# Kernel optimization log

Measured on AMD Instinct MI355X. Metric: run time of the kernel, lower is better.

Reference implementation:

```python
import jax, jax.numpy as jnp
import numpy as np

H, W = 512, 1024
NUM_CLASSES = 19
N_THING = 8
CENTER_THRESHOLD = 0.1
NMS_KERNEL = 7
KEEP_K = 128


def setup_inputs() -> dict:
    key = jax.random.key(0)
    k1, k2, k3 = jax.random.split(key, 3)
    return {
        "semantic_logits": jax.random.normal(k1, (1, H, W, NUM_CLASSES), jnp.float32),
        "center_heatmap": jax.random.uniform(k2, (H, W, 1), dtype=jnp.float32),
        "center_offsets": jax.random.normal(k3, (H, W, 2), jnp.float32) * 8.0,
        "thing_class_ids": jnp.arange(N_THING, dtype=jnp.int32),
    }


def _nms_heatmap(center_heatmap):
    # threshold, then keep only local maxima of a k x k max-pool (zero-padded;
    # -inf init is equivalent since thresholded values are >= 0)
    hm = jnp.where(center_heatmap > CENTER_THRESHOLD, center_heatmap, 0.0)  # [H,W,1]
    pooled = jax.lax.reduce_window(hm, -jnp.inf, jax.lax.max,
                                   (NMS_KERNEL, NMS_KERNEL, 1), (1, 1, 1), 'SAME')
    hm = jnp.where(pooled == hm, hm, 0.0)
    return hm[..., 0]  # [H,W]


def reference(semantic_logits, center_heatmap, center_offsets, thing_class_ids):
    # semantic prediction [H,W] (batch=1, like the TF merge path)
    semantic = jnp.argmax(semantic_logits, axis=-1).astype(jnp.int32)[0]
    thing_mask = (semantic[..., None] == thing_class_ids[None, None, :]).any(-1)  # [H,W] bool

    hm = _nms_heatmap(center_heatmap)                     # [H,W]
    scores, idx = jax.lax.top_k(hm.reshape(-1), KEEP_K)   # fixed-K centers
    valid = scores > 0.0                                  # [K]
    cy = (idx // W).astype(jnp.float32)
    cx = (idx % W).astype(jnp.float32)
    centers = jnp.stack([cy, cx], axis=-1)                # [K,2] (y,x)

    # center-per-pixel = pixel coord + predicted offset
    yy, xx = jnp.meshgrid(jnp.arange(H, dtype=jnp.float32),
                          jnp.arange(W, dtype=jnp.float32), indexing='ij')
    cpp = (jnp.stack([yy, xx], axis=-1) + center_offsets).reshape(-1, 2)  # [HW,2]

    # squared euclidean distance (argmin-equivalent to tf.norm), matmul form
    d2 = ((centers ** 2).sum(-1)[:, None]
          - 2.0 * centers @ cpp.T
          + (cpp ** 2).sum(-1)[None, :])                  # [K,HW]
    d2 = jnp.where(valid[:, None], d2, jnp.inf)           # mask padded centers
    assign = jnp.argmin(d2, axis=0).reshape(H, W)         # closest center index

    instance_seg = (assign.astype(jnp.int32) + 1) * thing_mask.astype(jnp.int32)
    score_map = scores[assign] * thing_mask.astype(jnp.float32)
    return instance_seg, hm, score_map, semantic
```

## Files before the change

kernel.cpp:

```cpp
#include <hip/hip_runtime.h>

#define HH 512
#define WW 1024
#define HWSZ (HH*WW)
#define NCLS 19
#define KEEP 128
#define CTHR 0.1f
#define NBLK 512
#define NRED 16
#define SEGPB 32
#define GSLOT 192
#define PRODOFF (1 + NRED)
typedef unsigned int u32;
typedef unsigned long long u64;

static __device__ __forceinline__ int key_bin2k(u64 k) {
    unsigned u = (unsigned)(k >> 32);
    if (u >= 0x3F000000u) {
        int b = 1024 + (int)((u - 0x3F000000u) >> 13);
        return b > 2047 ? 2047 : b;
    }
    return (int)(u >> 21);
}

static __device__ __forceinline__ int lds_push(int* cnt, bool want, int lane, u64 lmask_lt) {
    u64 mask = __ballot(want);
    int pos = -1;
    if (mask) {
        int leader = __builtin_ctzll(mask);
        int bpos = 0;
        if (lane == leader) bpos = atomicAdd(cnt, (int)__popcll(mask));
        bpos = __shfl(bpos, leader);
        if (want) pos = bpos + (int)__popcll(mask & lmask_lt);
    }
    return pos;
}

static __device__ __forceinline__ void bitonic_lds(u64* b, int m, int tid) {
    for (int kk = 2; kk <= m; kk <<= 1) {
        for (int j = kk >> 1; j; j >>= 1) {
            for (int i = tid; i < m; i += 256) {
                int ixj = i ^ j;
                if (ixj > i) {
                    bool desc = ((i & kk) == 0);
                    u64 a = b[i], c = b[ixj];
                    if ((a < c) == desc) { b[i] = c; b[ixj] = a; }
                }
            }
            __syncthreads();
        }
    }
}

static __device__ __forceinline__ void bitonic256_reg(u64* ov, int tid) {
    u64 a = ov[tid];
    __syncthreads();
    for (int kk = 2; kk <= 256; kk <<= 1) {
        bool desc = ((tid & kk) == 0);
        for (int j = kk >> 1; j; j >>= 1) {
            u64 b;
            if (j >= 64) {
                ov[tid] = a; __syncthreads();
                b = ov[tid ^ j]; __syncthreads();
            } else {
                b = __shfl_xor(a, j);
            }
            bool up = ((tid & j) == 0);
            bool keepMax = (up == desc);
            a = keepMax ? (a > b ? a : b) : (a < b ? a : b);
        }
    }
    ov[tid] = a;
    __syncthreads();
}

static __device__ __forceinline__ int cutoff2k(unsigned* hist, unsigned* cs, int tid,
                                               int* s_bin, int* s_K) {
    if (tid == 0) *s_bin = 2048;
    unsigned c = 0;
#pragma unroll
    for (int i = 0; i < 8; i++) c += hist[tid * 8 + i];
    cs[tid] = c;
    __syncthreads();
    for (int d = 1; d < 256; d <<= 1) {
        unsigned v = cs[tid];
        unsigned w = (tid + d < 256) ? cs[tid + d] : 0u;
        __syncthreads();
        cs[tid] = v + w;
        __syncthreads();
    }
    if (tid == 0) *s_K = (int)cs[0] < KEEP ? (int)cs[0] : KEEP;
    __syncthreads();
    int K = *s_K;
    unsigned above = (tid < 255) ? cs[tid + 1] : 0u;
    if (K > 0 && above < (unsigned)K && (unsigned)K <= cs[tid]) {
        unsigned acc = above;
        for (int b = 7; b >= 0; b--) {
            unsigned h = hist[tid * 8 + b];
            if (acc + h >= (unsigned)K) { *s_bin = tid * 8 + b; break; }
            acc += h;
        }
    }
    __syncthreads();
    return *s_bin;
}

__global__ void __launch_bounds__(256) pipeline_kernel(
        const float* __restrict__ heat, float* __restrict__ hm_out,
        u64* __restrict__ keys, u32* __restrict__ tagarr, u32* __restrict__ cntarr,
        u64* __restrict__ gtop, u32* __restrict__ gcnt, u32* __restrict__ tag2arr,
        int maxpb, float4* __restrict__ centers)
{
    __shared__ __align__(16) char smem[33792];
    __shared__ int scnt2[SEGPB];
    __shared__ int s_lcnt, s_m, s_bin, s_K, s_out;

    int tid = threadIdx.x, lane = tid & 63;
    u64 lmask_lt = (1ull << lane) - 1ull;

    if (blockIdx.x >= PRODOFF) {
        const int TX = 64, TY = 16;
        float* sin_ = (float*)smem;
        float* shm  = (float*)(smem + 6160);
        u64*   lk   = (u64*)(smem + 11792);
        int t = blockIdx.x - PRODOFF;
        if (tid == 0) s_lcnt = 0;
        int bx = t & 15, by = t >> 4;
        int ox = bx * TX, oy = by * TY;

        for (int i = tid; i < 22 * 70; i += 256) {
            int ly = i / 70, lx = i % 70;
            int gy = oy + ly - 3, gx = ox + lx - 3;
            float v = 0.f;
            if (gy >= 0 && gy < HH && gx >= 0 && gx < WW) {
                float tt = heat[gy * WW + gx];
                v = (tt > CTHR) ? tt : 0.f;
            }
            sin_[i] = v;
        }
        __syncthreads();
        for (int i = tid; i < 22 * 64; i += 256) {
            int ly = i >> 6, lx = i & 63;
            float m = sin_[ly * 70 + lx];
#pragma unroll
            for (int d = 1; d < 7; d++) m = fmaxf(m, sin_[ly * 70 + lx + d]);
            shm[i] = m;
        }
        __syncthreads();
        for (int i = tid; i < 16 * 64; i += 256) {
            int ly = i >> 6, lx = i & 63;
            float m = shm[i];
#pragma unroll
            for (int d = 1; d < 7; d++) m = fmaxf(m, shm[(ly + d) * 64 + lx]);
            float c = sin_[(ly + 3) * 70 + lx + 3];
            float o = (m == c) ? c : 0.f;
            int gy = oy + ly, gx = ox + lx;
            hm_out[gy * WW + gx] = o;
            if (o > 0.f) {
                int pos = atomicAdd(&s_lcnt, 1);
                lk[pos] = ((u64)__float_as_uint(o) << 32) |
                          (u64)(0xFFFFFFFFu - (unsigned)(gy * WW + gx));
            }
        }
        __syncthreads();
        int n = s_lcnt < maxpb ? s_lcnt : maxpb;
        for (int i = tid; i < n; i += 256)
            keys[(size_t)i * NBLK + t] = lk[i];
        __syncthreads();
        if (tid == 0) {
            __hip_atomic_store(&cntarr[t], (u32)n, __ATOMIC_RELAXED, __HIP_MEMORY_SCOPE_AGENT);
            __hip_atomic_store(&tagarr[t], 1u, __ATOMIC_RELEASE, __HIP_MEMORY_SCOPE_AGENT);
        }
        return;
    }

    u64* kbuf = (u64*)smem;
    unsigned* hist = (unsigned*)(smem + 24576);
    unsigned* cs   = (unsigned*)(smem + 32768);

    if (blockIdx.x >= 1) {
        int r = blockIdx.x - 1, g0 = r * SEGPB;
        if (tid < SEGPB) {
            while (__hip_atomic_load(&tagarr[g0 + tid], __ATOMIC_RELAXED,
                                     __HIP_MEMORY_SCOPE_AGENT) != 1u)
                __builtin_amdgcn_s_sleep(8);
        }
        __syncthreads();
        if (tid == 0) __threadfence();
        __syncthreads();
        if (tid < SEGPB) {
            int c = (int)cntarr[g0 + tid];
            scnt2[tid] = c < 0 ? 0 : (c > maxpb ? maxpb : c);
        }
        if (tid == 0) s_m = 0;
        { uint4* h4 = (uint4*)hist; for (int i = tid; i < 512; i += 256) h4[i] = make_uint4(0,0,0,0); }
        __syncthreads();
        int mxc = 0;
        for (int j = 0; j < SEGPB; j++) { int c = scnt2[j]; mxc = c > mxc ? c : mxc; }
        int nslots = SEGPB * mxc;

        for (int base = 0; base < nslots; base += 1024) {
            u64 kv[4]; bool pv[4];
#pragma unroll
            for (int u = 0; u < 4; u++) {
                int i = base + u * 256 + tid;
                int sg = i & (SEGPB - 1), sl = i >> 5;
                pv[u] = (i < nslots) && (sl < scnt2[sg]);
                kv[u] = pv[u] ? keys[(size_t)sl * NBLK + (g0 + sg)] : 0ull;
            }
#pragma unroll
            for (int u = 0; u < 4; u++)
                if (pv[u]) atomicAdd(&hist[key_bin2k(kv[u])], 1u);
        }
        __syncthreads();
        int cb = cutoff2k(hist, cs, tid, &s_bin, &s_K);

        for (int base = 0; base < nslots; base += 1024) {
#pragma unroll
            for (int u = 0; u < 4; u++) {
                int i = base + u * 256 + tid;
                int sg = i & (SEGPB - 1), sl = i >> 5;
                bool pv = (i < nslots) && (sl < scnt2[sg]);
                u64 kv = pv ? keys[(size_t)sl * NBLK + (g0 + sg)] : 0ull;
                bool want = pv && key_bin2k(kv) >= cb;
                int pos = lds_push(&s_m, want, lane, lmask_lt);
                if (want) kbuf[pos] = kv;
            }
        }
        __syncthreads();
        int n = s_m;
        if (n <= GSLOT) {
            for (int i = tid; i < n; i += 256) gtop[r * GSLOT + i] = kbuf[i];
            if (tid == 0) s_out = n;
        } else {
            int m = 256; while (m < n) m <<= 1;
            for (int i = tid; i < m; i += 256) if (i >= n) kbuf[i] = 0ull;
            __syncthreads();
            if (m == 256) bitonic256_reg(kbuf, tid); else bitonic_lds(kbuf, m, tid);
            if (tid < KEEP) gtop[r * GSLOT + tid] = kbuf[tid];
            if (tid == 0) s_out = KEEP;
        }
        __syncthreads();
        if (tid == 0) {
            __hip_atomic_store(&gcnt[r], (u32)s_out, __ATOMIC_RELAXED, __HIP_MEMORY_SCOPE_AGENT);
            __hip_atomic_store(&tag2arr[r], 1u, __ATOMIC_RELEASE, __HIP_MEMORY_SCOPE_AGENT);
        }
        return;
    }

    if (tid < NRED) {
        while (__hip_atomic_load(&tag2arr[tid], __ATOMIC_RELAXED,
                                 __HIP_MEMORY_SCOPE_AGENT) != 1u)
            __builtin_amdgcn_s_sleep(8);
    }
    __syncthreads();
    if (tid == 0) __threadfence();
    __syncthreads();
    if (tid < NRED) {
        int c = (int)gcnt[tid];
        scnt2[tid] = c < 0 ? 0 : (c > GSLOT ? GSLOT : c);
    }
    if (tid == 0) s_m = 0;
    { uint4* h4 = (uint4*)hist; for (int i = tid; i < 512; i += 256) h4[i] = make_uint4(0,0,0,0); }
    __syncthreads();

    const int nslots = NRED * GSLOT;
    for (int base = 0; base < nslots; base += 1024) {
        u64 kv[4]; bool pv[4];
#pragma unroll
        for (int u = 0; u < 4; u++) {
            int i = base + u * 256 + tid;
            int b = i / GSLOT, j = i - b * GSLOT;
            pv[u] = (j < scnt2[b]);
            kv[u] = pv[u] ? gtop[i] : 0ull;
        }
#pragma unroll
        for (int u = 0; u < 4; u++)
            if (pv[u]) atomicAdd(&hist[key_bin2k(kv[u])], 1u);
    }
    __syncthreads();
    int cb = cutoff2k(hist, cs, tid, &s_bin, &s_K);

    for (int base = 0; base < nslots; base += 1024) {
#pragma unroll
        for (int u = 0; u < 4; u++) {
            int i = base + u * 256 + tid;
            int b = i / GSLOT, j = i - b * GSLOT;
            bool pv = (j < scnt2[b]);
            u64 kv = pv ? gtop[i] : 0ull;
            bool want = pv && key_bin2k(kv) >= cb;
            int pos = lds_push(&s_m, want, lane, lmask_lt);
            if (want) kbuf[pos] = kv;
        }
    }
    __syncthreads();
    int n = s_m;
    int m = 256; while (m < n) m <<= 1;
    for (int i = tid; i < m; i += 256) if (i >= n) kbuf[i] = 0ull;
    __syncthreads();
    if (m == 256) bitonic256_reg(kbuf, tid); else bitonic_lds(kbuf, m, tid);

    if (tid < KEEP) {
        u64 k64 = kbuf[tid];
        float sc_, cy, cx, a;
        if (k64 == 0ull) { sc_ = 0.f; cy = 0.f; cx = 0.f; a = 0.f; }
        else {
            sc_ = __uint_as_float((unsigned)(k64 >> 32));
            unsigned idx = 0xFFFFFFFFu - (unsigned)(k64 & 0xFFFFFFFFu);
            cy = (float)(idx / WW);
            cx = (float)(idx % WW);
            a = cy * cy + cx * cx;
        }
        centers[tid] = make_float4(cy, cx, a, sc_);
    }
    __hip_atomic_store(&tagarr[2 * tid],     0u, __ATOMIC_RELAXED, __HIP_MEMORY_SCOPE_AGENT);
    __hip_atomic_store(&tagarr[2 * tid + 1], 0u, __ATOMIC_RELAXED, __HIP_MEMORY_SCOPE_AGENT);
    if (tid < NRED)
        __hip_atomic_store(&tag2arr[tid], 0u, __ATOMIC_RELAXED, __HIP_MEMORY_SCOPE_AGENT);
}

__global__ void __launch_bounds__(256) assign_kernel(
        const float* __restrict__ logits, const float* __restrict__ offs,
        const int* __restrict__ thing_ids, int n_thing,
        const float4* __restrict__ centers, float* __restrict__ out)
{
    __shared__ float4 sc[KEEP];
    __shared__ float4 skept[KEEP];
    __shared__ int   skidx[KEEP];
    __shared__ float slog[256 * NCLS];
    __shared__ float sred[16];
    __shared__ float ured[4];
    __shared__ int   wcnt[4];
    __shared__ int   s_nkept;
    __shared__ int   sids[32];

    int tid = threadIdx.x;
    if (tid < KEEP) sc[tid] = centers[tid];
    if (tid < n_thing) sids[tid] = thing_ids[tid];

    int bx = blockIdx.x & 63;
    int by = blockIdx.x >> 6;
    int lr = tid >> 4, lc = tid & 15;
    int gy = by * 16 + lr, gx = bx * 16 + lc;
    int p  = gy * WW + gx;

    {
        const float4* src4 = (const float4*)(logits + ((size_t)(by * 16) * WW + bx * 16) * NCLS);
        float4* dst4 = (float4*)slog;
        for (int i = tid; i < 16 * 76; i += 256) {
            int r = i / 76, cidx = i % 76;
            dst4[i] = src4[(size_t)r * 4864 + cidx];
        }
    }

    float2 off2 = ((const float2*)offs)[p];
    float py = __fadd_rn((float)gy, off2.x);
    float px = __fadd_rn((float)gx, off2.y);

    float ymn = py, ymx = py, xmn = px, xmx = px;
    for (int d = 32; d; d >>= 1) {
        ymn = fminf(ymn, __shfl_xor(ymn, d));
        ymx = fmaxf(ymx, __shfl_xor(ymx, d));
        xmn = fminf(xmn, __shfl_xor(xmn, d));
        xmx = fmaxf(xmx, __shfl_xor(xmx, d));
    }
    if ((tid & 63) == 0) {
        int w = tid >> 6;
        sred[w * 4 + 0] = ymn; sred[w * 4 + 1] = ymx;
        sred[w * 4 + 2] = xmn; sred[w * 4 + 3] = xmx;
    }
    __syncthreads();

    ymn = fminf(fminf(sred[0], sred[4]), fminf(sred[8],  sred[12]));
    ymx = fmaxf(fmaxf(sred[1], sred[5]), fmaxf(sred[9],  sred[13]));
    xmn = fminf(fminf(sred[2], sred[6]), fminf(sred[10], sred[14]));
    xmx = fmaxf(fmaxf(sred[3], sred[7]), fmaxf(sred[11], sred[15]));

    float L = INFINITY, U = INFINITY;
    bool valid = false;
    if (tid < KEEP) {
        float4 c4 = sc[tid];
        valid = (c4.w > 0.f);
        if (valid) {
            float dyl = fmaxf(fmaxf(ymn - c4.x, c4.x - ymx), 0.f);
            float dxl = fmaxf(fmaxf(xmn - c4.y, c4.y - xmx), 0.f);
            L = dyl * dyl + dxl * dxl;
            float dyu = fmaxf(fabsf(c4.x - ymn), fabsf(c4.x - ymx));
            float dxu = fmaxf(fabsf(c4.y - xmn), fabsf(c4.y - xmx));
            U = dyu * dyu + dxu * dxu;
        }
    }
    float u = U;
    for (int d = 32; d; d >>= 1) u = fminf(u, __shfl_xor(u, d));
    if ((tid & 63) == 0) ured[tid >> 6] = u;
    __syncthreads();
    float Umin = fminf(fminf(ured[0], ured[1]), fminf(ured[2], ured[3]));

    bool keep = valid && (L <= Umin + 8.0f);
    u64 mask = __ballot(keep);
    int lane = tid & 63;
    int prefix = __popcll(mask & ((1ull << lane) - 1ull));
    if (lane == 0) wcnt[tid >> 6] = __popcll(mask);
    __syncthreads();
    int base = (tid >> 6) == 1 ? wcnt[0] : 0;
    if (keep) { skept[base + prefix] = sc[tid]; skidx[base + prefix] = tid; }
    if (tid == 0) s_nkept = wcnt[0] + wcnt[1];
    __syncthreads();

    const float* l = slog + tid * NCLS;
    float best = l[0];
    int cls = 0;
#pragma unroll
    for (int cc = 1; cc < NCLS; cc++) {
        float v = l[cc];
        if (v > best) { best = v; cls = cc; }
    }
    bool thing = false;
    for (int j = 0; j < n_thing; j++) thing = thing || (cls == sids[j]);

    float b = __fadd_rn(__fmul_rn(py, py), __fmul_rn(px, px));

    float bestd = INFINITY;
    int bi = -1;
    int nk = s_nkept;
    for (int k = 0; k < nk; k++) {
        float4 c4 = skept[k];
        float m  = __fmaf_rn(c4.y, px, __fmul_rn(c4.x, py));
        float d2 = __fadd_rn(__fsub_rn(c4.z, __fadd_rn(m, m)), b);
        if (d2 < bestd) { bestd = d2; bi = k; }
    }

    float inst, smap;
    if (bi < 0) { inst = thing ? 1.f : 0.f; smap = 0.f; }
    else {
        inst = thing ? (float)(skidx[bi] + 1) : 0.f;
        smap = thing ? skept[bi].w : 0.f;
    }
    out[p] = inst;
    out[2 * HWSZ + p] = smap;
    out[3 * HWSZ + p] = (float)cls;
}

extern "C" void kernel_launch(void* const* d_in, const int* in_sizes, int n_in,
                              void* d_out, int out_size, void* d_ws, size_t ws_size,
                              hipStream_t stream) {
    const float* logits = (const float*)d_in[0];
    const float* heat   = (const float*)d_in[1];
    const float* offs   = (const float*)d_in[2];
    const int*   tids   = (const int*)d_in[3];
    int n_thing = in_sizes[3];
    if (n_thing > 32) n_thing = 32;

    float* out = (float*)d_out;
    char* ws = (char*)d_ws;
    u32* tagarr  = (u32*)ws;
    u32* tag2arr = (u32*)(ws + 2048);
    u32* cntarr  = (u32*)(ws + 4096);
    u32* gcnt    = (u32*)(ws + 6144);
    float4* centers = (float4*)(ws + 8192);
    u64* gtop = (u64*)(ws + 16384);
    long long avail = (long long)ws_size - 65536;
    int maxpb = (int)(avail / (NBLK * 8));
    if (maxpb > 96) maxpb = 96;
    if (maxpb < 16) maxpb = 16;
    u64* keys = (u64*)(ws + 65536);

    pipeline_kernel<<<dim3(NBLK + PRODOFF), dim3(256), 0, stream>>>(
        heat, out + HWSZ, keys, tagarr, cntarr, gtop, gcnt, tag2arr, maxpb, centers);
    assign_kernel<<<dim3(2048), dim3(256), 0, stream>>>(
        logits, offs, tids, n_thing, centers, out);
}
```

Measured before the change: 51.20 us.

## Fuse assign stage into producer blocks of a single persistent mega-kernel

```diff
diff --git a/kernel.cpp b/kernel.cpp
--- a/kernel.cpp
+++ b/kernel.cpp
@@ -10,7 +10,7 @@
 #define NRED 16
 #define SEGPB 32
 #define GSLOT 192
-#define PRODOFF (1 + NRED)
+#define WOFF (1 + NRED)
 typedef unsigned int u32;
 typedef unsigned long long u64;
 
@@ -105,26 +105,36 @@
     return *s_bin;
 }
 
-__global__ void __launch_bounds__(256) pipeline_kernel(
-        const float* __restrict__ heat, float* __restrict__ hm_out,
-        u64* __restrict__ keys, u32* __restrict__ tagarr, u32* __restrict__ cntarr,
+__global__ void __launch_bounds__(256) mega_kernel(
+        const float* __restrict__ logits, const float* __restrict__ heat,
+        const float* __restrict__ offs, const int* __restrict__ thing_ids, int n_thing,
+        float* __restrict__ out, u64* __restrict__ keys,
+        u32* __restrict__ tagarr, u32* __restrict__ cntarr,
         u64* __restrict__ gtop, u32* __restrict__ gcnt, u32* __restrict__ tag2arr,
-        int maxpb, float4* __restrict__ centers)
+        u32* __restrict__ wflags, u32* __restrict__ centersw, int maxpb)
 {
     __shared__ __align__(16) char smem[33792];
     __shared__ int scnt2[SEGPB];
-    __shared__ int s_lcnt, s_m, s_bin, s_K, s_out;
-
-    int tid = threadIdx.x, lane = tid & 63;
+    __shared__ int s_lcnt, s_m, s_bin, s_K, s_out, s_nkept;
+    __shared__ float sred[16];
+    __shared__ float ured[4];
+    __shared__ int wcnt[4];
+    __shared__ int sids[32];
+    __shared__ float4 sc[KEEP];
+    __shared__ float4 skept[KEEP];
+    __shared__ int skidx[KEEP];
+
+    int tid = threadIdx.x, lane = tid & 63, wid = tid >> 6;
     u64 lmask_lt = (1ull << lane) - 1ull;
 
-    if (blockIdx.x >= PRODOFF) {
+    if (blockIdx.x >= WOFF) {
         const int TX = 64, TY = 16;
         float* sin_ = (float*)smem;
         float* shm  = (float*)(smem + 6160);
         u64*   lk   = (u64*)(smem + 11792);
-        int t = blockIdx.x - PRODOFF;
+        int t = blockIdx.x - WOFF;
         if (tid == 0) s_lcnt = 0;
+        if (tid < n_thing) sids[tid] = thing_ids[tid];
         int bx = t & 15, by = t >> 4;
         int ox = bx * TX, oy = by * TY;
 
@@ -155,7 +165,7 @@
             float c = sin_[(ly + 3) * 70 + lx + 3];
             float o = (m == c) ? c : 0.f;
             int gy = oy + ly, gx = ox + lx;
-            hm_out[gy * WW + gx] = o;
+            out[HWSZ + gy * WW + gx] = o;
             if (o > 0.f) {
                 int pos = atomicAdd(&s_lcnt, 1);
                 lk[pos] = ((u64)__float_as_uint(o) << 32) |
@@ -170,6 +180,128 @@
         if (tid == 0) {
             __hip_atomic_store(&cntarr[t], (u32)n, __ATOMIC_RELAXED, __HIP_MEMORY_SCOPE_AGENT);
             __hip_atomic_store(&tagarr[t], 1u, __ATOMIC_RELEASE, __HIP_MEMORY_SCOPE_AGENT);
+        }
+
+        float* slog = (float*)smem;
+        for (int j = 0; j < 4; j++) {
+            int tile = t + NBLK * j;
+            __syncthreads();
+            int tbx = tile & 63, tby = tile >> 6;
+            int lr = tid >> 4, lc = tid & 15;
+            int gy = tby * 16 + lr, gx = tbx * 16 + lc;
+            int p = gy * WW + gx;
+
+            {
+                const float4* src4 = (const float4*)(logits + ((size_t)(tby * 16) * WW + tbx * 16) * NCLS);
+                float4* dst4 = (float4*)slog;
+                for (int i = tid; i < 16 * 76; i += 256) {
+                    int r = i / 76, cidx = i % 76;
+                    dst4[i] = src4[(size_t)r * 4864 + cidx];
+                }
+            }
+
+            float2 off2 = ((const float2*)offs)[p];
+            float py = __fadd_rn((float)gy, off2.x);
+            float px = __fadd_rn((float)gx, off2.y);
+
+            float ymn = py, ymx = py, xmn = px, xmx = px;
+            for (int d = 32; d; d >>= 1) {
+                ymn = fminf(ymn, __shfl_xor(ymn, d));
+                ymx = fmaxf(ymx, __shfl_xor(ymx, d));
+                xmn = fminf(xmn, __shfl_xor(xmn, d));
+                xmx = fmaxf(xmx, __shfl_xor(xmx, d));
+            }
+            if (lane == 0) {
+                sred[wid * 4 + 0] = ymn; sred[wid * 4 + 1] = ymx;
+                sred[wid * 4 + 2] = xmn; sred[wid * 4 + 3] = xmx;
+            }
+
+            if (j == 0) {
+                if (tid == 0) {
+                    u32* mf = wflags + (size_t)t * 4;
+                    while (__hip_atomic_load(mf, __ATOMIC_RELAXED, __HIP_MEMORY_SCOPE_AGENT) != 1u)
+                        __builtin_amdgcn_s_sleep(8);
+                    __hip_atomic_store(mf, 0u, __ATOMIC_RELAXED, __HIP_MEMORY_SCOPE_AGENT);
+                }
+                __syncthreads();
+                if (tid < KEEP) {
+                    u32 w0 = __hip_atomic_load(&centersw[tid * 4 + 0], __ATOMIC_RELAXED, __HIP_MEMORY_SCOPE_AGENT);
+                    u32 w1 = __hip_atomic_load(&centersw[tid * 4 + 1], __ATOMIC_RELAXED, __HIP_MEMORY_SCOPE_AGENT);
+                    u32 w2 = __hip_atomic_load(&centersw[tid * 4 + 2], __ATOMIC_RELAXED, __HIP_MEMORY_SCOPE_AGENT);
+                    u32 w3 = __hip_atomic_load(&centersw[tid * 4 + 3], __ATOMIC_RELAXED, __HIP_MEMORY_SCOPE_AGENT);
+                    sc[tid] = make_float4(__uint_as_float(w0), __uint_as_float(w1),
+                                          __uint_as_float(w2), __uint_as_float(w3));
+                }
+            }
+            __syncthreads();
+
+            float lymn = fminf(fminf(sred[0], sred[4]), fminf(sred[8],  sred[12]));
+            float lymx = fmaxf(fmaxf(sred[1], sred[5]), fmaxf(sred[9],  sred[13]));
+            float lxmn = fminf(fminf(sred[2], sred[6]), fminf(sred[10], sred[14]));
+            float lxmx = fmaxf(fmaxf(sred[3], sred[7]), fmaxf(sred[11], sred[15]));
+
+            float L = INFINITY, U = INFINITY;
+            bool valid = false;
+            if (tid < KEEP) {
+                float4 c4 = sc[tid];
+                valid = (c4.w > 0.f);
+                if (valid) {
+                    float dyl = fmaxf(fmaxf(lymn - c4.x, c4.x - lymx), 0.f);
+                    float dxl = fmaxf(fmaxf(lxmn - c4.y, c4.y - lxmx), 0.f);
+                    L = dyl * dyl + dxl * dxl;
+                    float dyu = fmaxf(fabsf(c4.x - lymn), fabsf(c4.x - lymx));
+                    float dxu = fmaxf(fabsf(c4.y - lxmn), fabsf(c4.y - lxmx));
+                    U = dyu * dyu + dxu * dxu;
+                }
+            }
+            float u = U;
+            for (int d = 32; d; d >>= 1) u = fminf(u, __shfl_xor(u, d));
+            if (lane == 0) ured[wid] = u;
+            __syncthreads();
+            float Umin = fminf(fminf(ured[0], ured[1]), fminf(ured[2], ured[3]));
+
+            bool keep = valid && (L <= Umin + 8.0f);
+            u64 kmask = __ballot(keep);
+            int prefix = __popcll(kmask & lmask_lt);
+            if (lane == 0) wcnt[wid] = __popcll(kmask);
+            __syncthreads();
+            int base = (wid == 1) ? wcnt[0] : 0;
+            if (keep) { skept[base + prefix] = sc[tid]; skidx[base + prefix] = tid; }
+            if (tid == 0) s_nkept = wcnt[0] + wcnt[1];
+            __syncthreads();
+
+            const float* l = slog + tid * NCLS;
+            float best = l[0];
+            int cls = 0;
+#pragma unroll
+            for (int cc = 1; cc < NCLS; cc++) {
+                float v = l[cc];
+                if (v > best) { best = v; cls = cc; }
+            }
+            bool thing = false;
+            for (int jj = 0; jj < n_thing; jj++) thing = thing || (cls == sids[jj]);
+
+            float b = __fadd_rn(__fmul_rn(py, py), __fmul_rn(px, px));
+
+            float bestd = INFINITY;
+            int bi = -1;
+            int nk = s_nkept;
+            for (int k = 0; k < nk; k++) {
+                float4 c4 = skept[k];
+                float m  = __fmaf_rn(c4.y, px, __fmul_rn(c4.x, py));
+                float d2 = __fadd_rn(__fsub_rn(c4.z, __fadd_rn(m, m)), b);
+                if (d2 < bestd) { bestd = d2; bi = k; }
+            }
+
+            float inst, smap;
+            if (bi < 0) { inst = thing ? 1.f : 0.f; smap = 0.f; }
+            else {
+                inst = thing ? (float)(skidx[bi] + 1) : 0.f;
+                smap = thing ? skept[bi].w : 0.f;
+            }
+            out[p] = inst;
+            out[2 * HWSZ + p] = smap;
+            out[3 * HWSZ + p] = (float)cls;
         }
         return;
     }
@@ -311,134 +443,18 @@
             cx = (float)(idx % WW);
             a = cy * cy + cx * cx;
         }
-        centers[tid] = make_float4(cy, cx, a, sc_);
-    }
+        __hip_atomic_store(&centersw[tid * 4 + 0], __float_as_uint(cy), __ATOMIC_RELAXED, __HIP_MEMORY_SCOPE_AGENT);
+        __hip_atomic_store(&centersw[tid * 4 + 1], __float_as_uint(cx), __ATOMIC_RELAXED, __HIP_MEMORY_SCOPE_AGENT);
+        __hip_atomic_store(&centersw[tid * 4 + 2], __float_as_uint(a),  __ATOMIC_RELAXED, __HIP_MEMORY_SCOPE_AGENT);
+        __hip_atomic_store(&centersw[tid * 4 + 3], __float_as_uint(sc_), __ATOMIC_RELAXED, __HIP_MEMORY_SCOPE_AGENT);
+    }
+    __syncthreads();
+    __hip_atomic_store(&wflags[(size_t)(2 * tid) * 4],     1u, __ATOMIC_RELAXED, __HIP_MEMORY_SCOPE_AGENT);
+    __hip_atomic_store(&wflags[(size_t)(2 * tid + 1) * 4], 1u, __ATOMIC_RELAXED, __HIP_MEMORY_SCOPE_AGENT);
     __hip_atomic_store(&tagarr[2 * tid],     0u, __ATOMIC_RELAXED, __HIP_MEMORY_SCOPE_AGENT);
     __hip_atomic_store(&tagarr[2 * tid + 1], 0u, __ATOMIC_RELAXED, __HIP_MEMORY_SCOPE_AGENT);
     if (tid < NRED)
         __hip_atomic_store(&tag2arr[tid], 0u, __ATOMIC_RELAXED, __HIP_MEMORY_SCOPE_AGENT);
-}
-
-__global__ void __launch_bounds__(256) assign_kernel(
-        const float* __restrict__ logits, const float* __restrict__ offs,
-        const int* __restrict__ thing_ids, int n_thing,
-        const float4* __restrict__ centers, float* __restrict__ out)
-{
-    __shared__ float4 sc[KEEP];
-    __shared__ float4 skept[KEEP];
-    __shared__ int   skidx[KEEP];
-    __shared__ float slog[256 * NCLS];
-    __shared__ float sred[16];
-    __shared__ float ured[4];
-    __shared__ int   wcnt[4];
-    __shared__ int   s_nkept;
-    __shared__ int   sids[32];
-
-    int tid = threadIdx.x;
-    if (tid < KEEP) sc[tid] = centers[tid];
-    if (tid < n_thing) sids[tid] = thing_ids[tid];
-
-    int bx = blockIdx.x & 63;
-    int by = blockIdx.x >> 6;
-    int lr = tid >> 4, lc = tid & 15;
-    int gy = by * 16 + lr, gx = bx * 16 + lc;
-    int p  = gy * WW + gx;
-
-    {
-        const float4* src4 = (const float4*)(logits + ((size_t)(by * 16) * WW + bx * 16) * NCLS);
-        float4* dst4 = (float4*)slog;
-        for (int i = tid; i < 16 * 76; i += 256) {
-            int r = i / 76, cidx = i % 76;
-            dst4[i] = src4[(size_t)r * 4864 + cidx];
-        }
-    }
-
-    float2 off2 = ((const float2*)offs)[p];
-    float py = __fadd_rn((float)gy, off2.x);
-    float px = __fadd_rn((float)gx, off2.y);
-
-    float ymn = py, ymx = py, xmn = px, xmx = px;
-    for (int d = 32; d; d >>= 1) {
-        ymn = fminf(ymn, __shfl_xor(ymn, d));
-        ymx = fmaxf(ymx, __shfl_xor(ymx, d));
-        xmn = fminf(xmn, __shfl_xor(xmn, d));
-        xmx = fmaxf(xmx, __shfl_xor(xmx, d));
-    }
-    if ((tid & 63) == 0) {
-        int w = tid >> 6;
-        sred[w * 4 + 0] = ymn; sred[w * 4 + 1] = ymx;
-        sred[w * 4 + 2] = xmn; sred[w * 4 + 3] = xmx;
-    }
-    __syncthreads();
-
-    ymn = fminf(fminf(sred[0], sred[4]), fminf(sred[8],  sred[12]));
-    ymx = fmaxf(fmaxf(sred[1], sred[5]), fmaxf(sred[9],  sred[13]));
-    xmn = fminf(fminf(sred[2], sred[6]), fminf(sred[10], sred[14]));
-    xmx = fmaxf(fmaxf(sred[3], sred[7]), fmaxf(sred[11], sred[15]));
-
-    float L = INFINITY, U = INFINITY;
-    bool valid = false;
-    if (tid < KEEP) {
-        float4 c4 = sc[tid];
-        valid = (c4.w > 0.f);
-        if (valid) {
-            float dyl = fmaxf(fmaxf(ymn - c4.x, c4.x - ymx), 0.f);
-            float dxl = fmaxf(fmaxf(xmn - c4.y, c4.y - xmx), 0.f);
-            L = dyl * dyl + dxl * dxl;
-            float dyu = fmaxf(fabsf(c4.x - ymn), fabsf(c4.x - ymx));
-            float dxu = fmaxf(fabsf(c4.y - xmn), fabsf(c4.y - xmx));
-            U = dyu * dyu + dxu * dxu;
-        }
-    }
-    float u = U;
-    for (int d = 32; d; d >>= 1) u = fminf(u, __shfl_xor(u, d));
-    if ((tid & 63) == 0) ured[tid >> 6] = u;
-    __syncthreads();
-    float Umin = fminf(fminf(ured[0], ured[1]), fminf(ured[2], ured[3]));
-
-    bool keep = valid && (L <= Umin + 8.0f);
-    u64 mask = __ballot(keep);
-    int lane = tid & 63;
-    int prefix = __popcll(mask & ((1ull << lane) - 1ull));
-    if (lane == 0) wcnt[tid >> 6] = __popcll(mask);
-    __syncthreads();
-    int base = (tid >> 6) == 1 ? wcnt[0] : 0;
-    if (keep) { skept[base + prefix] = sc[tid]; skidx[base + prefix] = tid; }
-    if (tid == 0) s_nkept = wcnt[0] + wcnt[1];
-    __syncthreads();
-
-    const float* l = slog + tid * NCLS;
-    float best = l[0];
-    int cls = 0;
-#pragma unroll
-    for (int cc = 1; cc < NCLS; cc++) {
-        float v = l[cc];
-        if (v > best) { best = v; cls = cc; }
-    }
-    bool thing = false;
-    for (int j = 0; j < n_thing; j++) thing = thing || (cls == sids[j]);
-
-    float b = __fadd_rn(__fmul_rn(py, py), __fmul_rn(px, px));
-
-    float bestd = INFINITY;
-    int bi = -1;
-    int nk = s_nkept;
-    for (int k = 0; k < nk; k++) {
-        float4 c4 = skept[k];
-        float m  = __fmaf_rn(c4.y, px, __fmul_rn(c4.x, py));
-        float d2 = __fadd_rn(__fsub_rn(c4.z, __fadd_rn(m, m)), b);
-        if (d2 < bestd) { bestd = d2; bi = k; }
-    }
-
-    float inst, smap;
-    if (bi < 0) { inst = thing ? 1.f : 0.f; smap = 0.f; }
-    else {
-        inst = thing ? (float)(skidx[bi] + 1) : 0.f;
-        smap = thing ? skept[bi].w : 0.f;
-    }
-    out[p] = inst;
-    out[2 * HWSZ + p] = smap;
-    out[3 * HWSZ + p] = (float)cls;
 }
 
 extern "C" void kernel_launch(void* const* d_in, const int* in_sizes, int n_in,
@@ -457,16 +473,16 @@
     u32* tag2arr = (u32*)(ws + 2048);
     u32* cntarr  = (u32*)(ws + 4096);
     u32* gcnt    = (u32*)(ws + 6144);
-    float4* centers = (float4*)(ws + 8192);
-    u64* gtop = (u64*)(ws + 16384);
+    u32* centersw = (u32*)(ws + 8192);
+    u32* wflags   = (u32*)(ws + 16384);
+    u64* gtop = (u64*)(ws + 24576);
     long long avail = (long long)ws_size - 65536;
     int maxpb = (int)(avail / (NBLK * 8));
     if (maxpb > 96) maxpb = 96;
     if (maxpb < 16) maxpb = 16;
     u64* keys = (u64*)(ws + 65536);
 
-    pipeline_kernel<<<dim3(NBLK + PRODOFF), dim3(256), 0, stream>>>(
-        heat, out + HWSZ, keys, tagarr, cntarr, gtop, gcnt, tag2arr, maxpb, centers);
-    assign_kernel<<<dim3(2048), dim3(256), 0, stream>>>(
-        logits, offs, tids, n_thing, centers, out);
-}
+    mega_kernel<<<dim3(NBLK + WOFF), dim3(256), 0, stream>>>(
+        logits, heat, offs, tids, n_thing, out, keys,
+        tagarr, cntarr, gtop, gcnt, tag2arr, wflags, centersw, maxpb);
+}
```

Measured after the change: 56.41 us. 1.1x slower.

## Split fused NMS/reduce pipeline into separate kernels instead of spin-wait tags

Applied to the files above, without the earlier changes.

```diff
diff --git a/kernel.cpp b/kernel.cpp
--- a/kernel.cpp
+++ b/kernel.cpp
@@ -10,7 +10,7 @@
 #define NRED 16
 #define SEGPB 32
 #define GSLOT 192
-#define PRODOFF (1 + NRED)
+#define TAGMAGIC 0x5A17EC0Du
 typedef unsigned int u32;
 typedef unsigned long long u64;
 
@@ -105,91 +105,80 @@
     return *s_bin;
 }
 
-__global__ void __launch_bounds__(256) pipeline_kernel(
-        const float* __restrict__ heat, float* __restrict__ hm_out,
-        u64* __restrict__ keys, u32* __restrict__ tagarr, u32* __restrict__ cntarr,
+__global__ void nms_kernel(const float* __restrict__ hm_in, float* __restrict__ hm_out,
+                           u64* __restrict__ keys, int* __restrict__ blkcnt, int maxpb)
+{
+    const int TX = 64, TY = 16;
+    __shared__ float sin_[TY + 6][TX + 6];
+    __shared__ float shm[TY + 6][TX];
+    __shared__ u64 lkeys[TX * TY];
+    __shared__ int lcnt;
+
+    if (threadIdx.x == 0) lcnt = 0;
+    int bx = blockIdx.x & 15, by = blockIdx.x >> 4;
+    int ox = bx * TX, oy = by * TY;
+
+    for (int i = threadIdx.x; i < (TY + 6) * (TX + 6); i += blockDim.x) {
+        int ly = i / (TX + 6), lx = i % (TX + 6);
+        int gy = oy + ly - 3, gx = ox + lx - 3;
+        float v = 0.f;
+        if (gy >= 0 && gy < HH && gx >= 0 && gx < WW) {
+            float t = hm_in[gy * WW + gx];
+            v = (t > CTHR) ? t : 0.f;
+        }
+        sin_[ly][lx] = v;
+    }
+    __syncthreads();
+    for (int i = threadIdx.x; i < (TY + 6) * TX; i += blockDim.x) {
+        int ly = i / TX, lx = i % TX;
+        float m = sin_[ly][lx];
+#pragma unroll
+        for (int d = 1; d < 7; d++) m = fmaxf(m, sin_[ly][lx + d]);
+        shm[ly][lx] = m;
+    }
+    __syncthreads();
+    for (int i = threadIdx.x; i < TY * TX; i += blockDim.x) {
+        int ly = i / TX, lx = i % TX;
+        float m = shm[ly][lx];
+#pragma unroll
+        for (int d = 1; d < 7; d++) m = fmaxf(m, shm[ly + d][lx]);
+        float c = sin_[ly + 3][lx + 3];
+        float o = (m == c) ? c : 0.f;
+        int gy = oy + ly, gx = ox + lx;
+        hm_out[gy * WW + gx] = o;
+        if (o > 0.f) {
+            int pos = atomicAdd(&lcnt, 1);
+            lkeys[pos] = ((u64)__float_as_uint(o) << 32) |
+                         (u64)(0xFFFFFFFFu - (unsigned)(gy * WW + gx));
+        }
+    }
+    __syncthreads();
+    int n = lcnt < maxpb ? lcnt : maxpb;
+    if (threadIdx.x == 0) blkcnt[blockIdx.x] = n;
+    for (int i = threadIdx.x; i < n; i += blockDim.x)
+        keys[(size_t)i * NBLK + blockIdx.x] = lkeys[i];
+}
+
+__global__ void __launch_bounds__(256) reduce_select_kernel(
+        const u64* __restrict__ keys, const int* __restrict__ blkcnt, int maxpb,
         u64* __restrict__ gtop, u32* __restrict__ gcnt, u32* __restrict__ tag2arr,
-        int maxpb, float4* __restrict__ centers)
+        float4* __restrict__ centers)
 {
     __shared__ __align__(16) char smem[33792];
     __shared__ int scnt2[SEGPB];
-    __shared__ int s_lcnt, s_m, s_bin, s_K, s_out;
+    __shared__ int s_m, s_bin, s_K, s_out;
 
     int tid = threadIdx.x, lane = tid & 63;
     u64 lmask_lt = (1ull << lane) - 1ull;
-
-    if (blockIdx.x >= PRODOFF) {
-        const int TX = 64, TY = 16;
-        float* sin_ = (float*)smem;
-        float* shm  = (float*)(smem + 6160);
-        u64*   lk   = (u64*)(smem + 11792);
-        int t = blockIdx.x - PRODOFF;
-        if (tid == 0) s_lcnt = 0;
-        int bx = t & 15, by = t >> 4;
-        int ox = bx * TX, oy = by * TY;
-
-        for (int i = tid; i < 22 * 70; i += 256) {
-            int ly = i / 70, lx = i % 70;
-            int gy = oy + ly - 3, gx = ox + lx - 3;
-            float v = 0.f;
-            if (gy >= 0 && gy < HH && gx >= 0 && gx < WW) {
-                float tt = heat[gy * WW + gx];
-                v = (tt > CTHR) ? tt : 0.f;
-            }
-            sin_[i] = v;
-        }
-        __syncthreads();
-        for (int i = tid; i < 22 * 64; i += 256) {
-            int ly = i >> 6, lx = i & 63;
-            float m = sin_[ly * 70 + lx];
-#pragma unroll
-            for (int d = 1; d < 7; d++) m = fmaxf(m, sin_[ly * 70 + lx + d]);
-            shm[i] = m;
-        }
-        __syncthreads();
-        for (int i = tid; i < 16 * 64; i += 256) {
-            int ly = i >> 6, lx = i & 63;
-            float m = shm[i];
-#pragma unroll
-            for (int d = 1; d < 7; d++) m = fmaxf(m, shm[(ly + d) * 64 + lx]);
-            float c = sin_[(ly + 3) * 70 + lx + 3];
-            float o = (m == c) ? c : 0.f;
-            int gy = oy + ly, gx = ox + lx;
-            hm_out[gy * WW + gx] = o;
-            if (o > 0.f) {
-                int pos = atomicAdd(&s_lcnt, 1);
-                lk[pos] = ((u64)__float_as_uint(o) << 32) |
-                          (u64)(0xFFFFFFFFu - (unsigned)(gy * WW + gx));
-            }
-        }
-        __syncthreads();
-        int n = s_lcnt < maxpb ? s_lcnt : maxpb;
-        for (int i = tid; i < n; i += 256)
-            keys[(size_t)i * NBLK + t] = lk[i];
-        __syncthreads();
-        if (tid == 0) {
-            __hip_atomic_store(&cntarr[t], (u32)n, __ATOMIC_RELAXED, __HIP_MEMORY_SCOPE_AGENT);
-            __hip_atomic_store(&tagarr[t], 1u, __ATOMIC_RELEASE, __HIP_MEMORY_SCOPE_AGENT);
-        }
-        return;
-    }
 
     u64* kbuf = (u64*)smem;
     unsigned* hist = (unsigned*)(smem + 24576);
     unsigned* cs   = (unsigned*)(smem + 32768);
 
-    if (blockIdx.x >= 1) {
-        int r = blockIdx.x - 1, g0 = r * SEGPB;
+    if (blockIdx.x < NRED) {
+        int r = blockIdx.x, g0 = r * SEGPB;
         if (tid < SEGPB) {
-            while (__hip_atomic_load(&tagarr[g0 + tid], __ATOMIC_RELAXED,
-                                     __HIP_MEMORY_SCOPE_AGENT) != 1u)
-                __builtin_amdgcn_s_sleep(8);
-        }
-        __syncthreads();
-        if (tid == 0) __threadfence();
-        __syncthreads();
-        if (tid < SEGPB) {
-            int c = (int)cntarr[g0 + tid];
+            int c = blkcnt[g0 + tid];
             scnt2[tid] = c < 0 ? 0 : (c > maxpb ? maxpb : c);
         }
         if (tid == 0) s_m = 0;
@@ -243,14 +232,14 @@
         __syncthreads();
         if (tid == 0) {
             __hip_atomic_store(&gcnt[r], (u32)s_out, __ATOMIC_RELAXED, __HIP_MEMORY_SCOPE_AGENT);
-            __hip_atomic_store(&tag2arr[r], 1u, __ATOMIC_RELEASE, __HIP_MEMORY_SCOPE_AGENT);
+            __hip_atomic_store(&tag2arr[r], TAGMAGIC, __ATOMIC_RELEASE, __HIP_MEMORY_SCOPE_AGENT);
         }
         return;
     }
 
     if (tid < NRED) {
         while (__hip_atomic_load(&tag2arr[tid], __ATOMIC_RELAXED,
-                                 __HIP_MEMORY_SCOPE_AGENT) != 1u)
+                                 __HIP_MEMORY_SCOPE_AGENT) != TAGMAGIC)
             __builtin_amdgcn_s_sleep(8);
     }
     __syncthreads();
@@ -313,8 +302,6 @@
         }
         centers[tid] = make_float4(cy, cx, a, sc_);
     }
-    __hip_atomic_store(&tagarr[2 * tid],     0u, __ATOMIC_RELAXED, __HIP_MEMORY_SCOPE_AGENT);
-    __hip_atomic_store(&tagarr[2 * tid + 1], 0u, __ATOMIC_RELAXED, __HIP_MEMORY_SCOPE_AGENT);
     if (tid < NRED)
         __hip_atomic_store(&tag2arr[tid], 0u, __ATOMIC_RELAXED, __HIP_MEMORY_SCOPE_AGENT);
 }
@@ -453,10 +440,9 @@
 
     float* out = (float*)d_out;
     char* ws = (char*)d_ws;
-    u32* tagarr  = (u32*)ws;
-    u32* tag2arr = (u32*)(ws + 2048);
-    u32* cntarr  = (u32*)(ws + 4096);
-    u32* gcnt    = (u32*)(ws + 6144);
+    u32* tag2arr = (u32*)ws;
+    u32* gcnt    = (u32*)(ws + 2048);
+    int* blkcnt  = (int*)(ws + 4096);
     float4* centers = (float4*)(ws + 8192);
     u64* gtop = (u64*)(ws + 16384);
     long long avail = (long long)ws_size - 65536;
@@ -465,8 +451,9 @@
     if (maxpb < 16) maxpb = 16;
     u64* keys = (u64*)(ws + 65536);
 
-    pipeline_kernel<<<dim3(NBLK + PRODOFF), dim3(256), 0, stream>>>(
-        heat, out + HWSZ, keys, tagarr, cntarr, gtop, gcnt, tag2arr, maxpb, centers);
+    nms_kernel<<<dim3(NBLK), dim3(256), 0, stream>>>(heat, out + HWSZ, keys, blkcnt, maxpb);
+    reduce_select_kernel<<<dim3(NRED + 1), dim3(256), 0, stream>>>(
+        keys, blkcnt, maxpb, gtop, gcnt, tag2arr, centers);
     assign_kernel<<<dim3(2048), dim3(256), 0, stream>>>(
         logits, offs, tids, n_thing, centers, out);
 }
```

Measured after the change: 42.69 us, median of 2. -16.6%, faster.
